# Kernel optimization log

Hardware: AMD Instinct MI355X
Metric: run time of the kernel (lower is better)

## Reference

```python
import jax, jax.numpy as jnp
import numpy as np

D_MODEL, D_STATE, D_CONV = 1024, 16, 4
B, T = 2, 2048


def setup_inputs() -> dict:
    key = jax.random.key(0)
    ks = jax.random.split(key, 8)
    x = jax.random.normal(ks[0], (B, T, D_MODEL), dtype=jnp.float32)
    in_proj_w = jax.random.normal(ks[1], (2 * D_MODEL, D_MODEL), dtype=jnp.float32) * 0.02
    conv_w = jax.random.normal(ks[2], (D_MODEL, 1, D_CONV), dtype=jnp.float32) * (1.0 / np.sqrt(D_CONV))
    conv_b = jnp.zeros((D_MODEL,), dtype=jnp.float32)
    x_proj_w = jax.random.normal(ks[3], (2 * D_STATE + 1, D_MODEL), dtype=jnp.float32) * (1.0 / np.sqrt(D_MODEL))
    dt_proj_w = jax.random.normal(ks[4], (D_MODEL, 1), dtype=jnp.float32)
    dt_proj_b = jax.random.normal(ks[5], (D_MODEL,), dtype=jnp.float32) * 0.1
    A_log = jnp.broadcast_to(jnp.log(jnp.arange(1, D_STATE + 1, dtype=jnp.float32))[None, :], (D_MODEL, D_STATE)).copy()
    out_proj_w = jax.random.normal(ks[6], (D_MODEL, D_MODEL), dtype=jnp.float32) * 0.02
    return {"x": x, "in_proj_w": in_proj_w, "conv_w": conv_w, "conv_b": conv_b,
            "x_proj_w": x_proj_w, "dt_proj_w": dt_proj_w, "dt_proj_b": dt_proj_b,
            "A_log": A_log, "out_proj_w": out_proj_w}


def _ssm_forward(x, in_proj_w, conv_w, conv_b, x_proj_w, dt_proj_w, dt_proj_b, A_log, out_proj_w):
    Bb, Tt, Dd = x.shape
    N = A_log.shape[1]
    # in_proj: [B,T,D] @ [D,2D]^T -> split into x_in, z
    xz = jnp.einsum('btd,ed->bte', x, in_proj_w)
    x_in, z = xz[..., :Dd], xz[..., Dd:]
    # causal depthwise conv1d (torch pads both sides then slices [:T] == left-pad only)
    x_c = jnp.swapaxes(x_in, 1, 2)  # [B,D,T]
    x_c = jax.lax.conv_general_dilated(
        x_c, conv_w, window_strides=(1,), padding=[(D_CONV - 1, 0)],
        feature_group_count=Dd, dimension_numbers=('NCH', 'OIH', 'NCH'))
    x_c = x_c + conv_b[None, :, None]
    x_conv = jax.nn.silu(jnp.swapaxes(x_c, 1, 2))  # [B,T,D]
    # selective parameters
    ssm_params = jnp.einsum('btd,ed->bte', x_conv, x_proj_w)  # [B,T,2N+1]
    B_ssm = ssm_params[..., :N]                 # [B,T,N]
    C_ssm = ssm_params[..., N:2 * N]            # [B,T,N]
    dt = jax.nn.softplus(ssm_params[..., -1:] * dt_proj_w[None, None, :, 0] + dt_proj_b)  # [B,T,D]
    A = -jnp.exp(A_log)                          # [D,N]
    dA = jnp.exp(dt[..., None] * A[None, None])                      # [B,T,D,N]
    dBx = dt[..., None] * B_ssm[:, :, None, :] * x_conv[..., None]   # [B,T,D,N]
    # sequential scan over T: h = dA*h + dBx ; y_t = sum_n h*C_t
    def step(h, inp):
        dA_t, dBx_t, C_t = inp  # [B,D,N],[B,D,N],[B,N]
        h = dA_t * h + dBx_t
        y_t = jnp.einsum('bdn,bn->bd', h, C_t)
        return h, y_t
    h0 = jnp.zeros((Bb, Dd, N), dtype=x.dtype)
    _, ys = jax.lax.scan(step, h0, (jnp.swapaxes(dA, 0, 1), jnp.swapaxes(dBx, 0, 1), jnp.swapaxes(C_ssm, 0, 1)))
    y = jnp.swapaxes(ys, 0, 1)  # [B,T,D]
    y = y * jax.nn.silu(z)
    return jnp.einsum('btd,ed->bte', y, out_proj_w)


def reference(x, in_proj_w, conv_w, conv_b, x_proj_w, dt_proj_w, dt_proj_b, A_log, out_proj_w):
    return _ssm_forward(x, in_proj_w, conv_w, conv_b, x_proj_w, dt_proj_w, dt_proj_b, A_log, out_proj_w)
```

## Files before the change

kernel.cpp:

```cpp
#include <hip/hip_runtime.h>
#include <stdint.h>

#define D_MODEL 1024
#define D_STATE 16
#define D_CONV  4
#define BB      2
#define TT      2048
#define M_ROWS  (BB * TT)
#define MiB     1048576ull
#define NCH     64
#define CHL     32

typedef short  short8 __attribute__((ext_vector_type(8)));
typedef __bf16 bf16x8 __attribute__((ext_vector_type(8)));
typedef float  f32x4  __attribute__((ext_vector_type(4)));

__device__ __forceinline__ float bf2f(unsigned short u) {
    union { unsigned int i; float f; } v; v.i = ((unsigned int)u) << 16; return v.f;
}
__device__ __forceinline__ unsigned short f2bf(float f) {
    union { float f; unsigned int i; } v; v.f = f;
    unsigned int r = v.i + 0x7fffu + ((v.i >> 16) & 1u);
    return (unsigned short)(r >> 16);
}
__device__ __forceinline__ float siluf(float v) {
    return v * __builtin_amdgcn_rcpf(1.f + __expf(-v));
}
__device__ __forceinline__ float softplusf(float x) {
    return (x > 20.f) ? x : __logf(1.f + __expf(x));
}
__device__ __forceinline__ void pow16(float p, float* o) {
    o[0]=p;          o[1]=p*p;        o[2]=o[1]*p;     o[3]=o[1]*o[1];
    o[4]=o[3]*p;     o[5]=o[3]*o[1];  o[6]=o[3]*o[2];  o[7]=o[3]*o[3];
    o[8]=o[7]*p;     o[9]=o[7]*o[1];  o[10]=o[7]*o[2]; o[11]=o[7]*o[3];
    o[12]=o[7]*o[4]; o[13]=o[7]*o[5]; o[14]=o[7]*o[6]; o[15]=o[7]*o[7];
}
__device__ __forceinline__ void gl_lds16(const unsigned short* g, unsigned short* l) {
    __builtin_amdgcn_global_load_lds(
        (const __attribute__((address_space(1))) unsigned int*)g,
        (__attribute__((address_space(3))) unsigned int*)(unsigned int)(uintptr_t)l,
        16, 0, 0);
}

__global__ __launch_bounds__(256) void cvt_k(
    const float* __restrict__ x, const float* __restrict__ wi,
    const float* __restrict__ wo, const float* __restrict__ xw,
    unsigned short* __restrict__ xb,  unsigned short* __restrict__ wib,
    unsigned short* __restrict__ wob, unsigned short* __restrict__ xwb)
{
    int g = blockIdx.x * blockDim.x + threadIdx.x;
    if (g >= 1843456) return;
    const float* src; unsigned short* dst; int off;
    if (g < 1048576)      { src = x;  dst = xb;  off = g; }
    else if (g < 1572864) { src = wi; dst = wib; off = g - 1048576; }
    else if (g < 1835008) { src = wo; dst = wob; off = g - 1572864; }
    else                  { src = xw; dst = xwb; off = g - 1835008; }
    float4 v = ((const float4*)src)[off];
    uint2 p;
    p.x = (unsigned int)f2bf(v.x) | ((unsigned int)f2bf(v.y) << 16);
    p.y = (unsigned int)f2bf(v.z) | ((unsigned int)f2bf(v.w) << 16);
    ((uint2*)dst)[off] = p;
}

template <int STORE_F32>
__global__ __launch_bounds__(256) void gemm_bt(
    const unsigned short* __restrict__ A,
    const unsigned short* __restrict__ W,
    void* __restrict__ dst0v,
    void* __restrict__ dst1v)
{
    constexpr int K = 1024, BK = 32;
    __shared__ unsigned short sA[128 * BK];
    __shared__ unsigned short sB[128 * BK];

    const int tid  = threadIdx.x;
    const int lane = tid & 63;
    const int wave = tid >> 6;
    const int wm = (wave & 1) * 64, wn = (wave >> 1) * 64;
    const int fm = lane & 15, quad = lane >> 4;
    const int bm = blockIdx.x * 128, bn = blockIdx.y * 128;

    void* dstv = (bn < 1024) ? dst0v : dst1v;
    const int bnl = (bn < 1024) ? bn : bn - 1024;

    const int sr = wave * 16 + (lane >> 2);
    const int c8 = (lane & 3) * 8;
    const unsigned short* gA = A + (size_t)(bm + sr) * K + c8;
    const unsigned short* gB = W + (size_t)(bn + sr) * K + c8;
    unsigned short* lA = sA + wave * 512;
    unsigned short* lB = sB + wave * 512;

    f32x4 acc[4][4] = {};

    for (int k0 = 0; k0 < K; k0 += BK) {
        gl_lds16(gA + k0,          lA);
        gl_lds16(gA + 64 * K + k0, lA + 2048);
        gl_lds16(gB + k0,          lB);
        gl_lds16(gB + 64 * K + k0, lB + 2048);
        __syncthreads();
        short8 af[4], bfr[4];
        #pragma unroll
        for (int i = 0; i < 4; ++i) {
            af[i]  = *(const short8*)&sA[(wm + i * 16 + fm) * BK + quad * 8];
            bfr[i] = *(const short8*)&sB[(wn + i * 16 + fm) * BK + quad * 8];
        }
        #pragma unroll
        for (int mi = 0; mi < 4; ++mi)
            #pragma unroll
            for (int ni = 0; ni < 4; ++ni)
                acc[mi][ni] = __builtin_amdgcn_mfma_f32_16x16x32_bf16(
                    __builtin_bit_cast(bf16x8, af[mi]),
                    __builtin_bit_cast(bf16x8, bfr[ni]),
                    acc[mi][ni], 0, 0, 0);
        __syncthreads();
    }

    #pragma unroll
    for (int mi = 0; mi < 4; ++mi) {
        #pragma unroll
        for (int ni = 0; ni < 4; ++ni) {
            int gm = bm + wm + mi * 16 + quad * 4;
            int gn = bnl + wn + ni * 16 + fm;
            #pragma unroll
            for (int rg = 0; rg < 4; ++rg) {
                if (STORE_F32)
                    ((float*)dstv)[(size_t)(gm + rg) * 1024 + gn] = acc[mi][ni][rg];
                else
                    ((unsigned short*)dstv)[(size_t)(gm + rg) * 1024 + gn] =
                        f2bf(acc[mi][ni][rg]);
            }
        }
    }
}

__global__ __launch_bounds__(64) void xproj_k(
    const unsigned short* __restrict__ xin,
    const unsigned short* __restrict__ xwb,
    const float* __restrict__ cw, const float* __restrict__ cb,
    float* __restrict__ sp)
{
    const int r0 = blockIdx.x * 2;
    const int t0 = r0 & (TT - 1);
    const int lane = threadIdx.x;
    const int dbase = lane * 16;

    float xr[5][16];
    #pragma unroll
    for (int k = 0; k < 5; ++k) {
        if (t0 - 3 + k >= 0) {
            const unsigned short* pr = xin + (size_t)(r0 - 3 + k) * D_MODEL + dbase;
            short8 v0 = *(const short8*)pr;
            short8 v1 = *(const short8*)(pr + 8);
            #pragma unroll
            for (int j = 0; j < 8; ++j) {
                xr[k][j]     = bf2f((unsigned short)v0[j]);
                xr[k][j + 8] = bf2f((unsigned short)v1[j]);
            }
        } else {
            #pragma unroll
            for (int j = 0; j < 16; ++j) xr[k][j] = 0.f;
        }
    }
    float xv0[16], xv1[16];
    #pragma unroll
    for (int j = 0; j < 16; ++j) {
        float4 w4 = *(const float4*)&cw[(dbase + j) * 4];
        float cbj = cb[dbase + j];
        float a0 = cbj + w4.x*xr[0][j] + w4.y*xr[1][j] + w4.z*xr[2][j] + w4.w*xr[3][j];
        float a1 = cbj + w4.x*xr[1][j] + w4.y*xr[2][j] + w4.z*xr[3][j] + w4.w*xr[4][j];
        xv0[j] = siluf(a0);
        xv1[j] = siluf(a1);
    }

    float A0[33], A1[33];
    #pragma unroll
    for (int e = 0; e < 33; ++e) {
        const unsigned short* wr = xwb + (size_t)e * D_MODEL + dbase;
        short8 w0 = *(const short8*)wr;
        short8 w1 = *(const short8*)(wr + 8);
        float a0 = 0.f, a1 = 0.f;
        #pragma unroll
        for (int j = 0; j < 8; ++j) {
            float wa = bf2f((unsigned short)w0[j]);
            float wb = bf2f((unsigned short)w1[j]);
            a0 += wa * xv0[j] + wb * xv0[j + 8];
            a1 += wa * xv1[j] + wb * xv1[j + 8];
        }
        A0[e] = a0; A1[e] = a1;
    }

    __shared__ float red0[64 * 33];
    __shared__ float red1[64 * 33];
    #pragma unroll
    for (int e = 0; e < 33; ++e) {
        red0[lane * 33 + e] = A0[e];
        red1[lane * 33 + e] = A1[e];
    }
    __syncthreads();
    if (lane < 33) {
        float y0 = 0.f, y1 = 0.f;
        for (int j = 0; j < 64; ++j) {
            y0 += red0[j * 33 + lane];
            y1 += red1[j * 33 + lane];
        }
        sp[(size_t)r0 * 33 + lane]       = y0;
        sp[(size_t)(r0 + 1) * 33 + lane] = y1;
    }
}

__global__ __launch_bounds__(256, 4) void scan_p1(
    const float* __restrict__ sp, const unsigned short* __restrict__ xin,
    const float* __restrict__ cw, const float* __restrict__ cb,
    const float* __restrict__ wdt, const float* __restrict__ bdt,
    float2* __restrict__ sm)
{
    const int tid = threadIdx.x;
    const int d0 = blockIdx.x * 256, d = d0 + tid;
    const int c = blockIdx.y, b = blockIdx.z;
    const size_t row0 = (size_t)b * TT + c * CHL;

    __shared__ float s_sp[CHL * 36];
    __shared__ unsigned short s_x[CHL * 256];
    for (int i = tid; i < CHL * 33; i += 256)
        s_sp[(i / 33) * 36 + (i % 33)] = sp[row0 * 33 + i];
    #pragma unroll
    for (int p = 0; p < CHL / 8; ++p) {
        int li = p * 256 + tid;
        int t = li >> 5, dg = (li & 31) * 8;
        *(uint4*)&s_x[t * 256 + dg] =
            *(const uint4*)&xin[(row0 + t) * D_MODEL + d0 + dg];
    }
    __syncthreads();

    const float4 k4 = *(const float4*)&cw[d * 4];
    const float kb = cb[d], wd = wdt[d], bd = bdt[d];
    float xm3 = 0.f, xm2 = 0.f, xm1 = 0.f;
    if (c != 0) {
        xm3 = bf2f(xin[(row0 - 3) * D_MODEL + d]);
        xm2 = bf2f(xin[(row0 - 2) * D_MODEL + d]);
        xm1 = bf2f(xin[(row0 - 1) * D_MODEL + d]);
    }

    float h[16] = {};
    float Sdt = 0.f;
    #pragma unroll 2
    for (int tl = 0; tl < CHL; ++tl) {
        float xcur = bf2f(s_x[tl * 256 + tid]);
        float a = kb + k4.x * xm3 + k4.y * xm2 + k4.z * xm1 + k4.w * xcur;
        xm3 = xm2; xm2 = xm1; xm1 = xcur;
        float xc = siluf(a);
        float dt = softplusf(s_sp[tl * 36 + 32] * wd + bd);
        Sdt += dt;
        float dtx = dt * xc;
        float dA[16];
        pow16(__expf(-dt), dA);
        float4 B0 = *(const float4*)&s_sp[tl * 36 + 0];
        float4 B1 = *(const float4*)&s_sp[tl * 36 + 4];
        float4 B2 = *(const float4*)&s_sp[tl * 36 + 8];
        float4 B3 = *(const float4*)&s_sp[tl * 36 + 12];
        float Bv[16] = {B0.x,B0.y,B0.z,B0.w, B1.x,B1.y,B1.z,B1.w,
                        B2.x,B2.y,B2.z,B2.w, B3.x,B3.y,B3.z,B3.w};
        #pragma unroll
        for (int n = 0; n < 16; ++n)
            h[n] = fmaf(dA[n], h[n], dtx * Bv[n]);
    }
    float qA[16];
    pow16(__expf(-Sdt), qA);
    size_t base = ((size_t)(b * NCH + c) * 16) * 1024 + d;
    #pragma unroll
    for (int n = 0; n < 16; ++n)
        sm[base + n * 1024] = make_float2(qA[n], h[n]);
}

__global__ __launch_bounds__(256) void scan_p2(float2* __restrict__ sm)
{
    int idx = blockIdx.x * 256 + threadIdx.x;
    int b = idx >> 14;
    int r = idx & 16383;
    float2* s = sm + (size_t)b * (NCH * 16384) + r;
    float H = 0.f;
    for (int c0 = 0; c0 < NCH; c0 += 16) {
        float2 v[16];
        #pragma unroll
        for (int j = 0; j < 16; ++j)
            v[j] = s[(size_t)(c0 + j) * 16384];
        #pragma unroll
        for (int j = 0; j < 16; ++j) {
            s[(size_t)(c0 + j) * 16384].y = H;
            H = fmaf(v[j].x, H, v[j].y);
        }
    }
}

__global__ __launch_bounds__(256, 4) void scan_p3(
    const float* __restrict__ sp, const unsigned short* __restrict__ xin,
    const unsigned short* __restrict__ zb,
    const float* __restrict__ cw, const float* __restrict__ cb,
    const float* __restrict__ wdt, const float* __restrict__ bdt,
    const float2* __restrict__ sm, unsigned short* __restrict__ yg)
{
    const int tid = threadIdx.x;
    const int d0 = blockIdx.x * 256, d = d0 + tid;
    const int c = blockIdx.y, b = blockIdx.z;
    const size_t row0 = (size_t)b * TT + c * CHL;

    __shared__ float s_sp[CHL * 36];
    __shared__ unsigned short s_x[CHL * 256];
    __shared__ unsigned short s_z[CHL * 256];
    __shared__ unsigned short s_y[CHL * 256];
    for (int i = tid; i < CHL * 33; i += 256)
        s_sp[(i / 33) * 36 + (i % 33)] = sp[row0 * 33 + i];
    #pragma unroll
    for (int p = 0; p < CHL / 8; ++p) {
        int li = p * 256 + tid;
        int t = li >> 5, dg = (li & 31) * 8;
        *(uint4*)&s_x[t * 256 + dg] =
            *(const uint4*)&xin[(row0 + t) * D_MODEL + d0 + dg];
        *(uint4*)&s_z[t * 256 + dg] =
            *(const uint4*)&zb[(row0 + t) * D_MODEL + d0 + dg];
    }
    __syncthreads();

    const float4 k4 = *(const float4*)&cw[d * 4];
    const float kb = cb[d], wd = wdt[d], bd = bdt[d];
    float xm3 = 0.f, xm2 = 0.f, xm1 = 0.f;
    if (c != 0) {
        xm3 = bf2f(xin[(row0 - 3) * D_MODEL + d]);
        xm2 = bf2f(xin[(row0 - 2) * D_MODEL + d]);
        xm1 = bf2f(xin[(row0 - 1) * D_MODEL + d]);
    }

    float h[16];
    size_t base = ((size_t)(b * NCH + c) * 16) * 1024 + d;
    #pragma unroll
    for (int n = 0; n < 16; ++n) h[n] = sm[base + n * 1024].y;

    #pragma unroll 2
    for (int tl = 0; tl < CHL; ++tl) {
        float xcur = bf2f(s_x[tl * 256 + tid]);
        float a = kb + k4.x * xm3 + k4.y * xm2 + k4.z * xm1 + k4.w * xcur;
        xm3 = xm2; xm2 = xm1; xm1 = xcur;
        float xc = siluf(a);
        float dt = softplusf(s_sp[tl * 36 + 32] * wd + bd);
        float dtx = dt * xc;
        float dA[16];
        pow16(__expf(-dt), dA);
        float4 B0 = *(const float4*)&s_sp[tl * 36 + 0];
        float4 B1 = *(const float4*)&s_sp[tl * 36 + 4];
        float4 B2 = *(const float4*)&s_sp[tl * 36 + 8];
        float4 B3 = *(const float4*)&s_sp[tl * 36 + 12];
        float4 C0 = *(const float4*)&s_sp[tl * 36 + 16];
        float4 C1 = *(const float4*)&s_sp[tl * 36 + 20];
        float4 C2 = *(const float4*)&s_sp[tl * 36 + 24];
        float4 C3 = *(const float4*)&s_sp[tl * 36 + 28];
        float Bv[16] = {B0.x,B0.y,B0.z,B0.w, B1.x,B1.y,B1.z,B1.w,
                        B2.x,B2.y,B2.z,B2.w, B3.x,B3.y,B3.z,B3.w};
        float Cv[16] = {C0.x,C0.y,C0.z,C0.w, C1.x,C1.y,C1.z,C1.w,
                        C2.x,C2.y,C2.z,C2.w, C3.x,C3.y,C3.z,C3.w};
        float y0 = 0.f, y1 = 0.f, y2 = 0.f, y3 = 0.f;
        #pragma unroll
        for (int n = 0; n < 16; n += 4) {
            h[n]   = fmaf(dA[n],   h[n],   dtx * Bv[n]);
            h[n+1] = fmaf(dA[n+1], h[n+1], dtx * Bv[n+1]);
            h[n+2] = fmaf(dA[n+2], h[n+2], dtx * Bv[n+2]);
            h[n+3] = fmaf(dA[n+3], h[n+3], dtx * Bv[n+3]);
            y0 = fmaf(Cv[n],   h[n],   y0);
            y1 = fmaf(Cv[n+1], h[n+1], y1);
            y2 = fmaf(Cv[n+2], h[n+2], y2);
            y3 = fmaf(Cv[n+3], h[n+3], y3);
        }
        float z = bf2f(s_z[tl * 256 + tid]);
        s_y[tl * 256 + tid] = f2bf((y0 + y1 + y2 + y3) * siluf(z));
    }
    __syncthreads();
    #pragma unroll
    for (int p = 0; p < CHL / 8; ++p) {
        int li = p * 256 + tid;
        int t = li >> 5, dg = (li & 31) * 8;
        *(uint4*)&yg[(row0 + t) * D_MODEL + d0 + dg] = *(uint4*)&s_y[t * 256 + dg];
    }
}

extern "C" void kernel_launch(void* const* d_in, const int* in_sizes, int n_in,
                              void* d_out, int out_size, void* d_ws, size_t ws_size,
                              hipStream_t stream)
{
    const float* x     = (const float*)d_in[0];
    const float* w_in  = (const float*)d_in[1];
    const float* cw    = (const float*)d_in[2];
    const float* cb    = (const float*)d_in[3];
    const float* xw    = (const float*)d_in[4];
    const float* wdt   = (const float*)d_in[5];
    const float* bdt   = (const float*)d_in[6];
    const float* w_out = (const float*)d_in[8];

    char* ws = (char*)d_ws;
    unsigned short* wob = (unsigned short*)(ws);
    unsigned short* zb  = (unsigned short*)(ws + 2 * MiB);
    unsigned short* xin = (unsigned short*)(ws + 10 * MiB);
    float*          sp  = (float*)(ws + 18 * MiB);
    unsigned short* yg  = (unsigned short*)(ws + 19 * MiB);
    unsigned short* xb  = (unsigned short*)(ws + 27 * MiB);
    unsigned short* wib = (unsigned short*)(ws + 35 * MiB);
    float2*         sm  = (float2*)(ws + 27 * MiB);
    unsigned short* xwb = (unsigned short*)(ws + 59 * MiB);

    dim3 blk(256);
    cvt_k<<<dim3(7201), blk, 0, stream>>>(x, w_in, w_out, xw, xb, wib, wob, xwb);
    gemm_bt<0><<<dim3(32, 16), blk, 0, stream>>>(xb, wib, xin, zb);
    xproj_k<<<dim3(M_ROWS / 2), dim3(64), 0, stream>>>(xin, xwb, cw, cb, sp);
    scan_p1<<<dim3(4, NCH, BB), blk, 0, stream>>>(sp, xin, cw, cb, wdt, bdt, sm);
    scan_p2<<<dim3(128), blk, 0, stream>>>(sm);
    scan_p3<<<dim3(4, NCH, BB), blk, 0, stream>>>(sp, xin, zb, cw, cb, wdt, bdt, sm, yg);
    gemm_bt<1><<<dim3(32, 8), blk, 0, stream>>>(yg, wob, d_out, nullptr);
}
```

Before: 196.5 us.

## Fuse three scan kernels with grid barriers; halve out-proj GEMM N tile

Merges scan_p1, scan_p2 and scan_p3 into one persistent kernel of 512 blocks. It uses atomic-counter grid barriers, reset in cvt_k, and keeps the shared-memory x/sp tiles and conv history across phases, so two launches and the reloads are gone. It also templates the GEMM on the N tile and uses 64 for the output projection, doubling its grid to 512 blocks for better CU occupancy. The grid barrier only works if all 512 blocks are co-resident, otherwise it deadlocks.

```diff
diff --git a/kernel.cpp b/kernel.cpp
--- a/kernel.cpp
+++ b/kernel.cpp
@@ -10,6 +10,7 @@
 #define MiB     1048576ull
 #define NCH     64
 #define CHL     32
+#define NBLK    512
 
 typedef short  short8 __attribute__((ext_vector_type(8)));
 typedef __bf16 bf16x8 __attribute__((ext_vector_type(8)));
@@ -41,15 +42,28 @@
         (__attribute__((address_space(3))) unsigned int*)(unsigned int)(uintptr_t)l,
         16, 0, 0);
 }
+__device__ __forceinline__ void gridbar(unsigned* cnt) {
+    __threadfence();
+    __syncthreads();
+    if (threadIdx.x == 0) {
+        __hip_atomic_fetch_add(cnt, 1u, __ATOMIC_ACQ_REL, __HIP_MEMORY_SCOPE_AGENT);
+        while (__hip_atomic_load(cnt, __ATOMIC_ACQUIRE, __HIP_MEMORY_SCOPE_AGENT) < NBLK)
+            __builtin_amdgcn_s_sleep(2);
+    }
+    __syncthreads();
+    __threadfence();
+}
 
 __global__ __launch_bounds__(256) void cvt_k(
     const float* __restrict__ x, const float* __restrict__ wi,
     const float* __restrict__ wo, const float* __restrict__ xw,
     unsigned short* __restrict__ xb,  unsigned short* __restrict__ wib,
-    unsigned short* __restrict__ wob, unsigned short* __restrict__ xwb)
+    unsigned short* __restrict__ wob, unsigned short* __restrict__ xwb,
+    unsigned* __restrict__ cnt)
 {
     int g = blockIdx.x * blockDim.x + threadIdx.x;
     if (g >= 1843456) return;
+    if (g == 0) { cnt[0] = 0u; cnt[1] = 0u; }
     const float* src; unsigned short* dst; int off;
     if (g < 1048576)      { src = x;  dst = xb;  off = g; }
     else if (g < 1572864) { src = wi; dst = wib; off = g - 1048576; }
@@ -62,23 +76,23 @@
     ((uint2*)dst)[off] = p;
 }
 
-template <int STORE_F32>
+template <int STORE_F32, int BN>
 __global__ __launch_bounds__(256) void gemm_bt(
     const unsigned short* __restrict__ A,
     const unsigned short* __restrict__ W,
     void* __restrict__ dst0v,
     void* __restrict__ dst1v)
 {
-    constexpr int K = 1024, BK = 32;
+    constexpr int K = 1024, BK = 32, NI = BN / 32;
     __shared__ unsigned short sA[128 * BK];
-    __shared__ unsigned short sB[128 * BK];
+    __shared__ unsigned short sB[BN * BK];
 
     const int tid  = threadIdx.x;
     const int lane = tid & 63;
     const int wave = tid >> 6;
-    const int wm = (wave & 1) * 64, wn = (wave >> 1) * 64;
+    const int wm = (wave & 1) * 64, wn = (wave >> 1) * (BN / 2);
     const int fm = lane & 15, quad = lane >> 4;
-    const int bm = blockIdx.x * 128, bn = blockIdx.y * 128;
+    const int bm = blockIdx.x * 128, bn = blockIdx.y * BN;
 
     void* dstv = (bn < 1024) ? dst0v : dst1v;
     const int bnl = (bn < 1024) ? bn : bn - 1024;
@@ -90,24 +104,26 @@
     unsigned short* lA = sA + wave * 512;
     unsigned short* lB = sB + wave * 512;
 
-    f32x4 acc[4][4] = {};
+    f32x4 acc[4][NI] = {};
 
     for (int k0 = 0; k0 < K; k0 += BK) {
         gl_lds16(gA + k0,          lA);
         gl_lds16(gA + 64 * K + k0, lA + 2048);
-        gl_lds16(gB + k0,          lB);
-        gl_lds16(gB + 64 * K + k0, lB + 2048);
+        #pragma unroll
+        for (int r = 0; r < BN / 64; ++r)
+            gl_lds16(gB + r * 64 * K + k0, lB + r * 2048);
         __syncthreads();
-        short8 af[4], bfr[4];
-        #pragma unroll
-        for (int i = 0; i < 4; ++i) {
+        short8 af[4], bfr[NI];
+        #pragma unroll
+        for (int i = 0; i < 4; ++i)
             af[i]  = *(const short8*)&sA[(wm + i * 16 + fm) * BK + quad * 8];
+        #pragma unroll
+        for (int i = 0; i < NI; ++i)
             bfr[i] = *(const short8*)&sB[(wn + i * 16 + fm) * BK + quad * 8];
-        }
         #pragma unroll
         for (int mi = 0; mi < 4; ++mi)
             #pragma unroll
-            for (int ni = 0; ni < 4; ++ni)
+            for (int ni = 0; ni < NI; ++ni)
                 acc[mi][ni] = __builtin_amdgcn_mfma_f32_16x16x32_bf16(
                     __builtin_bit_cast(bf16x8, af[mi]),
                     __builtin_bit_cast(bf16x8, bfr[ni]),
@@ -118,7 +134,7 @@
     #pragma unroll
     for (int mi = 0; mi < 4; ++mi) {
         #pragma unroll
-        for (int ni = 0; ni < 4; ++ni) {
+        for (int ni = 0; ni < NI; ++ni) {
             int gm = bm + wm + mi * 16 + quad * 4;
             int gn = bnl + wn + ni * 16 + fm;
             #pragma unroll
@@ -208,100 +224,18 @@
     }
 }
 
-__global__ __launch_bounds__(256, 4) void scan_p1(
+__global__ __launch_bounds__(256) void scan_fused(
     const float* __restrict__ sp, const unsigned short* __restrict__ xin,
+    const unsigned short* __restrict__ zb,
     const float* __restrict__ cw, const float* __restrict__ cb,
     const float* __restrict__ wdt, const float* __restrict__ bdt,
-    float2* __restrict__ sm)
+    float2* __restrict__ sm, unsigned short* __restrict__ yg,
+    unsigned* __restrict__ cnt)
 {
     const int tid = threadIdx.x;
     const int d0 = blockIdx.x * 256, d = d0 + tid;
     const int c = blockIdx.y, b = blockIdx.z;
-    const size_t row0 = (size_t)b * TT + c * CHL;
-
-    __shared__ float s_sp[CHL * 36];
-    __shared__ unsigned short s_x[CHL * 256];
-    for (int i = tid; i < CHL * 33; i += 256)
-        s_sp[(i / 33) * 36 + (i % 33)] = sp[row0 * 33 + i];
-    #pragma unroll
-    for (int p = 0; p < CHL / 8; ++p) {
-        int li = p * 256 + tid;
-        int t = li >> 5, dg = (li & 31) * 8;
-        *(uint4*)&s_x[t * 256 + dg] =
-            *(const uint4*)&xin[(row0 + t) * D_MODEL + d0 + dg];
-    }
-    __syncthreads();
-
-    const float4 k4 = *(const float4*)&cw[d * 4];
-    const float kb = cb[d], wd = wdt[d], bd = bdt[d];
-    float xm3 = 0.f, xm2 = 0.f, xm1 = 0.f;
-    if (c != 0) {
-        xm3 = bf2f(xin[(row0 - 3) * D_MODEL + d]);
-        xm2 = bf2f(xin[(row0 - 2) * D_MODEL + d]);
-        xm1 = bf2f(xin[(row0 - 1) * D_MODEL + d]);
-    }
-
-    float h[16] = {};
-    float Sdt = 0.f;
-    #pragma unroll 2
-    for (int tl = 0; tl < CHL; ++tl) {
-        float xcur = bf2f(s_x[tl * 256 + tid]);
-        float a = kb + k4.x * xm3 + k4.y * xm2 + k4.z * xm1 + k4.w * xcur;
-        xm3 = xm2; xm2 = xm1; xm1 = xcur;
-        float xc = siluf(a);
-        float dt = softplusf(s_sp[tl * 36 + 32] * wd + bd);
-        Sdt += dt;
-        float dtx = dt * xc;
-        float dA[16];
-        pow16(__expf(-dt), dA);
-        float4 B0 = *(const float4*)&s_sp[tl * 36 + 0];
-        float4 B1 = *(const float4*)&s_sp[tl * 36 + 4];
-        float4 B2 = *(const float4*)&s_sp[tl * 36 + 8];
-        float4 B3 = *(const float4*)&s_sp[tl * 36 + 12];
-        float Bv[16] = {B0.x,B0.y,B0.z,B0.w, B1.x,B1.y,B1.z,B1.w,
-                        B2.x,B2.y,B2.z,B2.w, B3.x,B3.y,B3.z,B3.w};
-        #pragma unroll
-        for (int n = 0; n < 16; ++n)
-            h[n] = fmaf(dA[n], h[n], dtx * Bv[n]);
-    }
-    float qA[16];
-    pow16(__expf(-Sdt), qA);
-    size_t base = ((size_t)(b * NCH + c) * 16) * 1024 + d;
-    #pragma unroll
-    for (int n = 0; n < 16; ++n)
-        sm[base + n * 1024] = make_float2(qA[n], h[n]);
-}
-
-__global__ __launch_bounds__(256) void scan_p2(float2* __restrict__ sm)
-{
-    int idx = blockIdx.x * 256 + threadIdx.x;
-    int b = idx >> 14;
-    int r = idx & 16383;
-    float2* s = sm + (size_t)b * (NCH * 16384) + r;
-    float H = 0.f;
-    for (int c0 = 0; c0 < NCH; c0 += 16) {
-        float2 v[16];
-        #pragma unroll
-        for (int j = 0; j < 16; ++j)
-            v[j] = s[(size_t)(c0 + j) * 16384];
-        #pragma unroll
-        for (int j = 0; j < 16; ++j) {
-            s[(size_t)(c0 + j) * 16384].y = H;
-            H = fmaf(v[j].x, H, v[j].y);
-        }
-    }
-}
-
-__global__ __launch_bounds__(256, 4) void scan_p3(
-    const float* __restrict__ sp, const unsigned short* __restrict__ xin,
-    const unsigned short* __restrict__ zb,
-    const float* __restrict__ cw, const float* __restrict__ cb,
-    const float* __restrict__ wdt, const float* __restrict__ bdt,
-    const float2* __restrict__ sm, unsigned short* __restrict__ yg)
-{
-    const int tid = threadIdx.x;
-    const int d0 = blockIdx.x * 256, d = d0 + tid;
-    const int c = blockIdx.y, b = blockIdx.z;
+    const int flat = blockIdx.x + 4 * (blockIdx.y + NCH * blockIdx.z);
     const size_t row0 = (size_t)b * TT + c * CHL;
 
     __shared__ float s_sp[CHL * 36];
@@ -323,61 +257,120 @@
 
     const float4 k4 = *(const float4*)&cw[d * 4];
     const float kb = cb[d], wd = wdt[d], bd = bdt[d];
-    float xm3 = 0.f, xm2 = 0.f, xm1 = 0.f;
+    float bx3 = 0.f, bx2 = 0.f, bx1 = 0.f;
     if (c != 0) {
-        xm3 = bf2f(xin[(row0 - 3) * D_MODEL + d]);
-        xm2 = bf2f(xin[(row0 - 2) * D_MODEL + d]);
-        xm1 = bf2f(xin[(row0 - 1) * D_MODEL + d]);
-    }
-
-    float h[16];
-    size_t base = ((size_t)(b * NCH + c) * 16) * 1024 + d;
-    #pragma unroll
-    for (int n = 0; n < 16; ++n) h[n] = sm[base + n * 1024].y;
-
-    #pragma unroll 2
-    for (int tl = 0; tl < CHL; ++tl) {
-        float xcur = bf2f(s_x[tl * 256 + tid]);
-        float a = kb + k4.x * xm3 + k4.y * xm2 + k4.z * xm1 + k4.w * xcur;
-        xm3 = xm2; xm2 = xm1; xm1 = xcur;
-        float xc = siluf(a);
-        float dt = softplusf(s_sp[tl * 36 + 32] * wd + bd);
-        float dtx = dt * xc;
-        float dA[16];
-        pow16(__expf(-dt), dA);
-        float4 B0 = *(const float4*)&s_sp[tl * 36 + 0];
-        float4 B1 = *(const float4*)&s_sp[tl * 36 + 4];
-        float4 B2 = *(const float4*)&s_sp[tl * 36 + 8];
-        float4 B3 = *(const float4*)&s_sp[tl * 36 + 12];
-        float4 C0 = *(const float4*)&s_sp[tl * 36 + 16];
-        float4 C1 = *(const float4*)&s_sp[tl * 36 + 20];
-        float4 C2 = *(const float4*)&s_sp[tl * 36 + 24];
-        float4 C3 = *(const float4*)&s_sp[tl * 36 + 28];
-        float Bv[16] = {B0.x,B0.y,B0.z,B0.w, B1.x,B1.y,B1.z,B1.w,
-                        B2.x,B2.y,B2.z,B2.w, B3.x,B3.y,B3.z,B3.w};
-        float Cv[16] = {C0.x,C0.y,C0.z,C0.w, C1.x,C1.y,C1.z,C1.w,
-                        C2.x,C2.y,C2.z,C2.w, C3.x,C3.y,C3.z,C3.w};
-        float y0 = 0.f, y1 = 0.f, y2 = 0.f, y3 = 0.f;
-        #pragma unroll
-        for (int n = 0; n < 16; n += 4) {
-            h[n]   = fmaf(dA[n],   h[n],   dtx * Bv[n]);
-            h[n+1] = fmaf(dA[n+1], h[n+1], dtx * Bv[n+1]);
-            h[n+2] = fmaf(dA[n+2], h[n+2], dtx * Bv[n+2]);
-            h[n+3] = fmaf(dA[n+3], h[n+3], dtx * Bv[n+3]);
-            y0 = fmaf(Cv[n],   h[n],   y0);
-            y1 = fmaf(Cv[n+1], h[n+1], y1);
-            y2 = fmaf(Cv[n+2], h[n+2], y2);
-            y3 = fmaf(Cv[n+3], h[n+3], y3);
-        }
-        float z = bf2f(s_z[tl * 256 + tid]);
-        s_y[tl * 256 + tid] = f2bf((y0 + y1 + y2 + y3) * siluf(z));
-    }
-    __syncthreads();
-    #pragma unroll
-    for (int p = 0; p < CHL / 8; ++p) {
-        int li = p * 256 + tid;
-        int t = li >> 5, dg = (li & 31) * 8;
-        *(uint4*)&yg[(row0 + t) * D_MODEL + d0 + dg] = *(uint4*)&s_y[t * 256 + dg];
+        bx3 = bf2f(xin[(row0 - 3) * D_MODEL + d]);
+        bx2 = bf2f(xin[(row0 - 2) * D_MODEL + d]);
+        bx1 = bf2f(xin[(row0 - 1) * D_MODEL + d]);
+    }
+
+    {
+        float xm3 = bx3, xm2 = bx2, xm1 = bx1;
+        float h[16] = {};
+        float Sdt = 0.f;
+        #pragma unroll 2
+        for (int tl = 0; tl < CHL; ++tl) {
+            float xcur = bf2f(s_x[tl * 256 + tid]);
+            float a = kb + k4.x * xm3 + k4.y * xm2 + k4.z * xm1 + k4.w * xcur;
+            xm3 = xm2; xm2 = xm1; xm1 = xcur;
+            float xc = siluf(a);
+            float dt = softplusf(s_sp[tl * 36 + 32] * wd + bd);
+            Sdt += dt;
+            float dtx = dt * xc;
+            float dA[16];
+            pow16(__expf(-dt), dA);
+            float4 B0 = *(const float4*)&s_sp[tl * 36 + 0];
+            float4 B1 = *(const float4*)&s_sp[tl * 36 + 4];
+            float4 B2 = *(const float4*)&s_sp[tl * 36 + 8];
+            float4 B3 = *(const float4*)&s_sp[tl * 36 + 12];
+            float Bv[16] = {B0.x,B0.y,B0.z,B0.w, B1.x,B1.y,B1.z,B1.w,
+                            B2.x,B2.y,B2.z,B2.w, B3.x,B3.y,B3.z,B3.w};
+            #pragma unroll
+            for (int n = 0; n < 16; ++n)
+                h[n] = fmaf(dA[n], h[n], dtx * Bv[n]);
+        }
+        float qA[16];
+        pow16(__expf(-Sdt), qA);
+        size_t base = ((size_t)(b * NCH + c) * 16) * 1024 + d;
+        #pragma unroll
+        for (int n = 0; n < 16; ++n)
+            sm[base + n * 1024] = make_float2(qA[n], h[n]);
+    }
+
+    gridbar(&cnt[0]);
+
+    if (flat < 128) {
+        int idx = flat * 256 + tid;
+        int b2 = idx >> 14;
+        int r = idx & 16383;
+        float2* s = sm + (size_t)b2 * (NCH * 16384) + r;
+        float H = 0.f;
+        for (int c0 = 0; c0 < NCH; c0 += 16) {
+            float2 v[16];
+            #pragma unroll
+            for (int j = 0; j < 16; ++j)
+                v[j] = s[(size_t)(c0 + j) * 16384];
+            #pragma unroll
+            for (int j = 0; j < 16; ++j) {
+                s[(size_t)(c0 + j) * 16384].y = H;
+                H = fmaf(v[j].x, H, v[j].y);
+            }
+        }
+    }
+
+    gridbar(&cnt[1]);
+
+    {
+        float h[16];
+        size_t base = ((size_t)(b * NCH + c) * 16) * 1024 + d;
+        #pragma unroll
+        for (int n = 0; n < 16; ++n) h[n] = sm[base + n * 1024].y;
+
+        float xm3 = bx3, xm2 = bx2, xm1 = bx1;
+        #pragma unroll 2
+        for (int tl = 0; tl < CHL; ++tl) {
+            float xcur = bf2f(s_x[tl * 256 + tid]);
+            float a = kb + k4.x * xm3 + k4.y * xm2 + k4.z * xm1 + k4.w * xcur;
+            xm3 = xm2; xm2 = xm1; xm1 = xcur;
+            float xc = siluf(a);
+            float dt = softplusf(s_sp[tl * 36 + 32] * wd + bd);
+            float dtx = dt * xc;
+            float dA[16];
+            pow16(__expf(-dt), dA);
+            float4 B0 = *(const float4*)&s_sp[tl * 36 + 0];
+            float4 B1 = *(const float4*)&s_sp[tl * 36 + 4];
+            float4 B2 = *(const float4*)&s_sp[tl * 36 + 8];
+            float4 B3 = *(const float4*)&s_sp[tl * 36 + 12];
+            float4 C0 = *(const float4*)&s_sp[tl * 36 + 16];
+            float4 C1 = *(const float4*)&s_sp[tl * 36 + 20];
+            float4 C2 = *(const float4*)&s_sp[tl * 36 + 24];
+            float4 C3 = *(const float4*)&s_sp[tl * 36 + 28];
+            float Bv[16] = {B0.x,B0.y,B0.z,B0.w, B1.x,B1.y,B1.z,B1.w,
+                            B2.x,B2.y,B2.z,B2.w, B3.x,B3.y,B3.z,B3.w};
+            float Cv[16] = {C0.x,C0.y,C0.z,C0.w, C1.x,C1.y,C1.z,C1.w,
+                            C2.x,C2.y,C2.z,C2.w, C3.x,C3.y,C3.z,C3.w};
+            float y0 = 0.f, y1 = 0.f, y2 = 0.f, y3 = 0.f;
+            #pragma unroll
+            for (int n = 0; n < 16; n += 4) {
+                h[n]   = fmaf(dA[n],   h[n],   dtx * Bv[n]);
+                h[n+1] = fmaf(dA[n+1], h[n+1], dtx * Bv[n+1]);
+                h[n+2] = fmaf(dA[n+2], h[n+2], dtx * Bv[n+2]);
+                h[n+3] = fmaf(dA[n+3], h[n+3], dtx * Bv[n+3]);
+                y0 = fmaf(Cv[n],   h[n],   y0);
+                y1 = fmaf(Cv[n+1], h[n+1], y1);
+                y2 = fmaf(Cv[n+2], h[n+2], y2);
+                y3 = fmaf(Cv[n+3], h[n+3], y3);
+            }
+            float z = bf2f(s_z[tl * 256 + tid]);
+            s_y[tl * 256 + tid] = f2bf((y0 + y1 + y2 + y3) * siluf(z));
+        }
+        __syncthreads();
+        #pragma unroll
+        for (int p = 0; p < CHL / 8; ++p) {
+            int li = p * 256 + tid;
+            int t = li >> 5, dg = (li & 31) * 8;
+            *(uint4*)&yg[(row0 + t) * D_MODEL + d0 + dg] = *(uint4*)&s_y[t * 256 + dg];
+        }
     }
 }
 
@@ -404,13 +397,13 @@
     unsigned short* wib = (unsigned short*)(ws + 35 * MiB);
     float2*         sm  = (float2*)(ws + 27 * MiB);
     unsigned short* xwb = (unsigned short*)(ws + 59 * MiB);
+    unsigned*       cnt = (unsigned*)(ws + 60 * MiB);
 
     dim3 blk(256);
-    cvt_k<<<dim3(7201), blk, 0, stream>>>(x, w_in, w_out, xw, xb, wib, wob, xwb);
-    gemm_bt<0><<<dim3(32, 16), blk, 0, stream>>>(xb, wib, xin, zb);
+    cvt_k<<<dim3(7201), blk, 0, stream>>>(x, w_in, w_out, xw, xb, wib, wob, xwb, cnt);
+    gemm_bt<0, 128><<<dim3(32, 16), blk, 0, stream>>>(xb, wib, xin, zb);
     xproj_k<<<dim3(M_ROWS / 2), dim3(64), 0, stream>>>(xin, xwb, cw, cb, sp);
-    scan_p1<<<dim3(4, NCH, BB), blk, 0, stream>>>(sp, xin, cw, cb, wdt, bdt, sm);
-    scan_p2<<<dim3(128), blk, 0, stream>>>(sm);
-    scan_p3<<<dim3(4, NCH, BB), blk, 0, stream>>>(sp, xin, zb, cw, cb, wdt, bdt, sm, yg);
-    gemm_bt<1><<<dim3(32, 8), blk, 0, stream>>>(yg, wob, d_out, nullptr);
-}
+    scan_fused<<<dim3(4, NCH, BB), blk, 0, stream>>>(sp, xin, zb, cw, cb, wdt, bdt,
+                                                     sm, yg, cnt);
+    gemm_bt<1, 64><<<dim3(32, 16), blk, 0, stream>>>(yg, wob, d_out, nullptr);
+}
```

Result: slower. 456.4 us (+132.3%).
